# Kernel tuning notes

Hardware: AMD Instinct MI355X
Metric: run time of the kernel (lower is better)

## Reference

```python
import math
import jax, jax.numpy as jnp
import numpy as np

S = 4096          # total packed tokens (b*s with bsz=1)
NUM_HEADS = 16
HEAD_DIM = 80
SCALE = 1.0 / math.sqrt(HEAD_DIM)


def setup_inputs() -> dict:
    key = jax.random.key(0)
    kq, kk, kv = jax.random.split(key, 3)
    q = jax.random.normal(kq, (S, NUM_HEADS, HEAD_DIM), dtype=jnp.float32)
    k = jax.random.normal(kk, (S, NUM_HEADS, HEAD_DIM), dtype=jnp.float32)
    v = jax.random.normal(kv, (S, NUM_HEADS, HEAD_DIM), dtype=jnp.float32)
    # 4 packed sequences of 1024 tokens each (flatten_batch=True, bsz=1)
    cu_seqlens = jnp.array([0, 1024, 2048, 3072, 4096], dtype=jnp.int32)
    return {"q": q, "k": k, "v": v, "bsz": 1, "cu_seqlens": cu_seqlens}


def reference(q, k, v, bsz, cu_seqlens):
    # q/k/v: [(b s), h, d]; flatten_batch=True so bsz == 1
    s = q.shape[0] // bsz
    h, d = q.shape[1], q.shape[2]

    # Block-diagonal mask from cu_seqlens: True inside each packed sequence.
    seg = jnp.searchsorted(cu_seqlens[1:], jnp.arange(s), side="right")  # [s]
    mask = seg[:, None] == seg[None, :]                                  # [s, s]

    # '(b s) h d -> b h s d'
    qb = q.reshape(bsz, s, h, d).transpose(0, 2, 1, 3)
    kb = k.reshape(bsz, s, h, d).transpose(0, 2, 1, 3)
    vb = v.reshape(bsz, s, h, d).transpose(0, 2, 1, 3)

    scores = jnp.einsum("bhsd,bhtd->bhst", qb, kb) * SCALE
    bias = jnp.where(mask, jnp.zeros((), scores.dtype), jnp.finfo(scores.dtype).min)
    attn = jax.nn.softmax((scores + bias).astype(jnp.float32), axis=-1).astype(q.dtype)

    out = jnp.einsum("bhst,bhtd->bhsd", attn, vb)
    # 'b h s d -> (b s) h d'
    return out.transpose(0, 2, 1, 3).reshape(bsz * s, h, d)
```

## Files before the change

kernel.cpp:

```cpp
#include <hip/hip_runtime.h>
#include <hip/hip_bf16.h>
#include <math.h>

#define NTOK 4096
#define NH 16
#define HD 80
#define TOKSTRIDE (NH * HD)
#define QBLK 64
#define KVBLK 64
#define KSTR 80
#define VSTR 72
#define PSTR 72

typedef __bf16 bf16x4 __attribute__((ext_vector_type(4)));
typedef __bf16 bf16x8 __attribute__((ext_vector_type(8)));
typedef float  f32x4  __attribute__((ext_vector_type(4)));

__global__ __launch_bounds__(256)
void prepack(const float* __restrict__ qg, const float* __restrict__ kg,
             const float* __restrict__ vg, __bf16* __restrict__ qb,
             __bf16* __restrict__ kb, __bf16* __restrict__ vtb) {
  __shared__ __align__(16) __bf16 Vl[HD][VSTR];
  const int tid  = threadIdx.x;
  const int tok0 = blockIdx.x * 64;
  const int h    = blockIdx.y;
  const float qscale = 1.4426950408889634f / sqrtf((float)HD);

  for (int i = tid; i < 64 * 20; i += 256) {
    const int row = i / 20;
    const int c4  = (i % 20) * 4;
    const size_t gsrc = (size_t)(tok0 + row) * TOKSTRIDE + h * HD + c4;
    const size_t gdst = ((size_t)h * NTOK + tok0 + row) * HD + c4;

    float4 fq = *reinterpret_cast<const float4*>(qg + gsrc);
    bf16x4 uq;
    uq[0] = (__bf16)(fq.x * qscale); uq[1] = (__bf16)(fq.y * qscale);
    uq[2] = (__bf16)(fq.z * qscale); uq[3] = (__bf16)(fq.w * qscale);
    *reinterpret_cast<bf16x4*>(qb + gdst) = uq;

    float4 fk = *reinterpret_cast<const float4*>(kg + gsrc);
    bf16x4 uk;
    uk[0] = (__bf16)fk.x; uk[1] = (__bf16)fk.y;
    uk[2] = (__bf16)fk.z; uk[3] = (__bf16)fk.w;
    *reinterpret_cast<bf16x4*>(kb + gdst) = uk;

    float4 fv = *reinterpret_cast<const float4*>(vg + gsrc);
    Vl[c4 + 0][row] = (__bf16)fv.x; Vl[c4 + 1][row] = (__bf16)fv.y;
    Vl[c4 + 2][row] = (__bf16)fv.z; Vl[c4 + 3][row] = (__bf16)fv.w;
  }
  __syncthreads();
  for (int i = tid; i < HD * 8; i += 256) {
    const int d  = i / 8;
    const int c8 = (i % 8) * 8;
    bf16x8 val = *reinterpret_cast<const bf16x8*>(&Vl[d][c8]);
    *reinterpret_cast<bf16x8*>(vtb + ((size_t)h * HD + d) * NTOK + tok0 + c8) = val;
  }
}

__global__ __launch_bounds__(256, 4)
void vis_attn9(const __bf16* __restrict__ qb, const __bf16* __restrict__ kb,
               const __bf16* __restrict__ vtb, const int* __restrict__ cu,
               int n_cu, float* __restrict__ outg) {
  __shared__ __align__(16) unsigned char smem[31136];
  __bf16* Kl = reinterpret_cast<__bf16*>(smem);
  __bf16* Vt = reinterpret_cast<__bf16*>(smem + 10400);
  __bf16* Pl = reinterpret_cast<__bf16*>(smem + 21920);

  const int tid  = threadIdx.x;
  const int w    = tid >> 6;
  const int lane = tid & 63;
  const int lr   = lane & 15;
  const int g    = lane >> 4;

  const int q0 = blockIdx.x * QBLK;
  const int h  = blockIdx.y;

  int kv_start = 0, kv_end = NTOK;
  for (int i = 0; i + 1 < n_cu; ++i) {
    int a = cu[i], b = cu[i + 1];
    if (q0 >= a && q0 < b) { kv_start = a; kv_end = b; }
  }

  if (tid < 16) Kl[KVBLK * KSTR + tid] = (__bf16)0.0f;

  const int qrow = q0 + w * 16 + lr;
  const __bf16* qrptr = qb + ((size_t)h * NTOK + qrow) * HD;
  bf16x8 qf[3];
  #pragma unroll
  for (int c = 0; c < 3; ++c) {
    const int dbase = c * 32 + g * 8;
    if (dbase < HD) {
      qf[c] = *reinterpret_cast<const bf16x8*>(qrptr + dbase);
    } else {
      #pragma unroll
      for (int j = 0; j < 8; ++j) qf[c][j] = (__bf16)0.0f;
    }
  }

  bf16x8 vfl;
  {
    const __bf16 o = (lr == 0) ? (__bf16)1.0f : (__bf16)0.0f;
    #pragma unroll
    for (int j = 0; j < 8; ++j) vfl[j] = o;
  }

  f32x4 O[6];
  #pragma unroll
  for (int n = 0; n < 6; ++n) O[n] = (f32x4){0.f, 0.f, 0.f, 0.f};

  const __bf16* kbh  = kb  + (size_t)h * NTOK * HD;
  const __bf16* vtbh = vtb + (size_t)h * HD * NTOK;
  const char* gbase = reinterpret_cast<const char*>(kbh);
  const int vdelta = (int)(reinterpret_cast<const char*>(vtbh) - gbase);

  int goff[5], ginc[5], ldsoff[5];
  #pragma unroll
  for (int j = 0; j < 5; ++j) {
    const int c = tid + j * 256;
    if (c < 640) {
      const int row = c / 10, col = (c % 10) * 8;
      goff[j]   = (kv_start * HD + row * HD + col) * 2;
      ginc[j]   = KVBLK * HD * 2;
      ldsoff[j] = (row * KSTR + col) * 2;
    } else {
      const int c2 = c - 640, d = c2 / 8, kc = (c2 % 8) * 8;
      goff[j]   = vdelta + (kv_start + d * NTOK + kc) * 2;
      ginc[j]   = KVBLK * 2;
      ldsoff[j] = 10400 + (d * VSTR + kc) * 2;
    }
  }

  bf16x8 st[5];
  #pragma unroll
  for (int j = 0; j < 5; ++j) {
    st[j] = *reinterpret_cast<const bf16x8*>(gbase + goff[j]);
    goff[j] += ginc[j];
  }

  for (int kv0 = kv_start; kv0 < kv_end; kv0 += KVBLK) {
    __syncthreads();
    #pragma unroll
    for (int j = 0; j < 5; ++j)
      *reinterpret_cast<bf16x8*>(smem + ldsoff[j]) = st[j];
    __syncthreads();

    if (kv0 + KVBLK < kv_end) {
      #pragma unroll
      for (int j = 0; j < 5; ++j) {
        st[j] = *reinterpret_cast<const bf16x8*>(gbase + goff[j]);
        goff[j] += ginc[j];
      }
    }

    f32x4 S[4];
    __builtin_amdgcn_s_setprio(1);
    #pragma unroll
    for (int t = 0; t < 4; ++t) {
      S[t] = (f32x4){0.f, 0.f, 0.f, 0.f};
      #pragma unroll
      for (int c = 0; c < 3; ++c) {
        bf16x8 kf = *reinterpret_cast<const bf16x8*>(&Kl[(t * 16 + lr) * KSTR + c * 32 + g * 8]);
        S[t] = __builtin_amdgcn_mfma_f32_16x16x32_bf16(qf[c], kf, S[t], 0, 0, 0);
      }
    }
    __builtin_amdgcn_s_setprio(0);

    #pragma unroll
    for (int t = 0; t < 4; ++t) {
      #pragma unroll
      for (int r = 0; r < 4; ++r)
        S[t][r] = exp2f(S[t][r]);
    }

    #pragma unroll
    for (int t = 0; t < 4; ++t) {
      #pragma unroll
      for (int r = 0; r < 4; ++r)
        Pl[(w * 16 + g * 4 + r) * PSTR + t * 16 + lr] = (__bf16)S[t][r];
    }

    #pragma unroll
    for (int kc = 0; kc < 2; ++kc) {
      bf16x8 pf = *reinterpret_cast<const bf16x8*>(&Pl[(w * 16 + lr) * PSTR + kc * 32 + g * 8]);
      __builtin_amdgcn_s_setprio(1);
      #pragma unroll
      for (int n = 0; n < 5; ++n) {
        bf16x8 vf = *reinterpret_cast<const bf16x8*>(&Vt[(n * 16 + lr) * VSTR + kc * 32 + g * 8]);
        O[n] = __builtin_amdgcn_mfma_f32_16x16x32_bf16(pf, vf, O[n], 0, 0, 0);
      }
      O[5] = __builtin_amdgcn_mfma_f32_16x16x32_bf16(pf, vfl, O[5], 0, 0, 0);
      __builtin_amdgcn_s_setprio(0);
    }
  }

  float inv[4];
  #pragma unroll
  for (int r = 0; r < 4; ++r) {
    float l = __shfl(O[5][r], lane & 48);
    inv[r] = 1.0f / l;
  }
  const int orow0 = q0 + w * 16 + g * 4;
  #pragma unroll
  for (int n = 0; n < 5; ++n) {
    #pragma unroll
    for (int r = 0; r < 4; ++r)
      outg[(size_t)(orow0 + r) * TOKSTRIDE + h * HD + n * 16 + lr] = O[n][r] * inv[r];
  }
}

__global__ __launch_bounds__(256, 4)
void vis_attn_fb(const float* __restrict__ qg, const float* __restrict__ kg,
                 const float* __restrict__ vg, const int* __restrict__ cu,
                 int n_cu, float* __restrict__ outg) {
  __shared__ __align__(16) __bf16 Kl[KVBLK][104];
  __shared__ __align__(16) __bf16 Vt[HD][72];
  __shared__ __align__(16) __bf16 Pl[64][72];

  const int tid  = threadIdx.x;
  const int w    = tid >> 6;
  const int lane = tid & 63;
  const int lr   = lane & 15;
  const int g    = lane >> 4;
  const int q0 = blockIdx.x * 64;
  const int h  = blockIdx.y;

  int kv_start = 0, kv_end = NTOK;
  for (int i = 0; i + 1 < n_cu; ++i) {
    int a = cu[i], b = cu[i + 1];
    if (q0 >= a && q0 < b) { kv_start = a; kv_end = b; }
  }
  for (int i = tid; i < KVBLK * 16; i += 256)
    Kl[i >> 4][HD + (i & 15)] = (__bf16)0.0f;

  const float qscale = 1.4426950408889634f / sqrtf((float)HD);
  const int qrow = q0 + w * 16 + lr;
  const float* qptr = qg + (size_t)qrow * TOKSTRIDE + h * HD;
  bf16x8 qf[3];
  #pragma unroll
  for (int c = 0; c < 3; ++c) {
    const int dbase = c * 32 + g * 8;
    if (dbase < HD) {
      float4 f0 = *reinterpret_cast<const float4*>(qptr + dbase);
      float4 f1 = *reinterpret_cast<const float4*>(qptr + dbase + 4);
      qf[c][0] = (__bf16)(f0.x * qscale); qf[c][1] = (__bf16)(f0.y * qscale);
      qf[c][2] = (__bf16)(f0.z * qscale); qf[c][3] = (__bf16)(f0.w * qscale);
      qf[c][4] = (__bf16)(f1.x * qscale); qf[c][5] = (__bf16)(f1.y * qscale);
      qf[c][6] = (__bf16)(f1.z * qscale); qf[c][7] = (__bf16)(f1.w * qscale);
    } else {
      #pragma unroll
      for (int j = 0; j < 8; ++j) qf[c][j] = (__bf16)0.0f;
    }
  }

  f32x4 O[5];
  #pragma unroll
  for (int n = 0; n < 5; ++n) O[n] = (f32x4){0.f, 0.f, 0.f, 0.f};
  float m_run[4] = {-1e30f, -1e30f, -1e30f, -1e30f};
  float l_run[4] = {0.f, 0.f, 0.f, 0.f};

  for (int kv0 = kv_start; kv0 < kv_end; kv0 += KVBLK) {
    __syncthreads();
    for (int i = tid; i < KVBLK * (HD / 4); i += 256) {
      const int row = i / (HD / 4);
      const int c4  = (i % (HD / 4)) * 4;
      float4 f = *reinterpret_cast<const float4*>(
          kg + (size_t)(kv0 + row) * TOKSTRIDE + h * HD + c4);
      Kl[row][c4 + 0] = (__bf16)f.x; Kl[row][c4 + 1] = (__bf16)f.y;
      Kl[row][c4 + 2] = (__bf16)f.z; Kl[row][c4 + 3] = (__bf16)f.w;
    }
    for (int i = tid; i < KVBLK * (HD / 4); i += 256) {
      const int row = i / (HD / 4);
      const int c4  = (i % (HD / 4)) * 4;
      float4 f = *reinterpret_cast<const float4*>(
          vg + (size_t)(kv0 + row) * TOKSTRIDE + h * HD + c4);
      Vt[c4 + 0][row] = (__bf16)f.x; Vt[c4 + 1][row] = (__bf16)f.y;
      Vt[c4 + 2][row] = (__bf16)f.z; Vt[c4 + 3][row] = (__bf16)f.w;
    }
    __syncthreads();

    f32x4 S[4];
    #pragma unroll
    for (int t = 0; t < 4; ++t) {
      S[t] = (f32x4){0.f, 0.f, 0.f, 0.f};
      #pragma unroll
      for (int c = 0; c < 3; ++c) {
        bf16x8 kf = *reinterpret_cast<const bf16x8*>(&Kl[t * 16 + lr][c * 32 + g * 8]);
        S[t] = __builtin_amdgcn_mfma_f32_16x16x32_bf16(qf[c], kf, S[t], 0, 0, 0);
      }
    }
    float pmax[4];
    #pragma unroll
    for (int r = 0; r < 4; ++r)
      pmax[r] = fmaxf(fmaxf(S[0][r], S[1][r]), fmaxf(S[2][r], S[3][r]));
    #pragma unroll
    for (int r = 0; r < 4; ++r) {
      pmax[r] = fmaxf(pmax[r], __shfl_xor(pmax[r], 1));
      pmax[r] = fmaxf(pmax[r], __shfl_xor(pmax[r], 2));
      pmax[r] = fmaxf(pmax[r], __shfl_xor(pmax[r], 4));
      pmax[r] = fmaxf(pmax[r], __shfl_xor(pmax[r], 8));
    }
    float alpha[4];
    #pragma unroll
    for (int r = 0; r < 4; ++r) {
      float mn = fmaxf(m_run[r], pmax[r]);
      alpha[r] = exp2f(m_run[r] - mn);
      m_run[r] = mn;
    }
    #pragma unroll
    for (int t = 0; t < 4; ++t) {
      #pragma unroll
      for (int r = 0; r < 4; ++r)
        S[t][r] = exp2f(S[t][r] - m_run[r]);
    }
    float rsum[4];
    #pragma unroll
    for (int r = 0; r < 4; ++r) {
      rsum[r] = (S[0][r] + S[1][r]) + (S[2][r] + S[3][r]);
      rsum[r] += __shfl_xor(rsum[r], 1);
      rsum[r] += __shfl_xor(rsum[r], 2);
      rsum[r] += __shfl_xor(rsum[r], 4);
      rsum[r] += __shfl_xor(rsum[r], 8);
      l_run[r] = l_run[r] * alpha[r] + rsum[r];
    }
    #pragma unroll
    for (int n = 0; n < 5; ++n) {
      #pragma unroll
      for (int r = 0; r < 4; ++r) O[n][r] *= alpha[r];
    }
    #pragma unroll
    for (int t = 0; t < 4; ++t) {
      #pragma unroll
      for (int r = 0; r < 4; ++r)
        Pl[w * 16 + g * 4 + r][t * 16 + lr] = (__bf16)S[t][r];
    }
    #pragma unroll
    for (int kc = 0; kc < 2; ++kc) {
      bf16x8 pf = *reinterpret_cast<const bf16x8*>(&Pl[w * 16 + lr][kc * 32 + g * 8]);
      #pragma unroll
      for (int n = 0; n < 5; ++n) {
        bf16x8 vf = *reinterpret_cast<const bf16x8*>(&Vt[n * 16 + lr][kc * 32 + g * 8]);
        O[n] = __builtin_amdgcn_mfma_f32_16x16x32_bf16(pf, vf, O[n], 0, 0, 0);
      }
    }
  }

  float inv[4];
  #pragma unroll
  for (int r = 0; r < 4; ++r) inv[r] = 1.0f / l_run[r];
  const int orow0 = q0 + w * 16 + g * 4;
  #pragma unroll
  for (int n = 0; n < 5; ++n) {
    #pragma unroll
    for (int r = 0; r < 4; ++r)
      outg[(size_t)(orow0 + r) * TOKSTRIDE + h * HD + n * 16 + lr] = O[n][r] * inv[r];
  }
}

extern "C" void kernel_launch(void* const* d_in, const int* in_sizes, int n_in,
                              void* d_out, int out_size, void* d_ws, size_t ws_size,
                              hipStream_t stream) {
  const float* q  = (const float*)d_in[0];
  const float* k  = (const float*)d_in[1];
  const float* v  = (const float*)d_in[2];
  const int* cu   = (const int*)d_in[4];
  const int n_cu  = in_sizes[4];
  float* out      = (float*)d_out;

  const size_t one = (size_t)NH * NTOK * HD * sizeof(__bf16);

  if (ws_size >= 3 * one) {
    __bf16* qb  = (__bf16*)d_ws;
    __bf16* kb  = (__bf16*)((char*)d_ws + one);
    __bf16* vtb = (__bf16*)((char*)d_ws + 2 * one);
    dim3 gp(NTOK / 64, NH);
    prepack<<<gp, 256, 0, stream>>>(q, k, v, qb, kb, vtb);
    dim3 ga(NTOK / QBLK, NH);
    vis_attn9<<<ga, 256, 0, stream>>>(qb, kb, vtb, cu, n_cu, out);
  } else {
    dim3 gf(NTOK / 64, NH);
    vis_attn_fb<<<gf, 256, 0, stream>>>(q, k, v, cu, n_cu, out);
  }
}
```

Before: 64.26 us.

## Split KV tile across wave pairs and reduce partial outputs via LDS

New measurement: 65.12 us. No clear change (+1.3%).

```diff
diff --git a/kernel.cpp b/kernel.cpp
--- a/kernel.cpp
+++ b/kernel.cpp
@@ -57,17 +57,20 @@
   }
 }
 
-__global__ __launch_bounds__(256, 4)
-void vis_attn9(const __bf16* __restrict__ qb, const __bf16* __restrict__ kb,
-               const __bf16* __restrict__ vtb, const int* __restrict__ cu,
-               int n_cu, float* __restrict__ outg) {
+__global__ __launch_bounds__(512, 2)
+void vis_attn10(const __bf16* __restrict__ qb, const __bf16* __restrict__ kb,
+                const __bf16* __restrict__ vtb, const int* __restrict__ cu,
+                int n_cu, float* __restrict__ outg) {
   __shared__ __align__(16) unsigned char smem[31136];
   __bf16* Kl = reinterpret_cast<__bf16*>(smem);
   __bf16* Vt = reinterpret_cast<__bf16*>(smem + 10400);
   __bf16* Pl = reinterpret_cast<__bf16*>(smem + 21920);
+  float*  Cx = reinterpret_cast<float*>(smem);
 
   const int tid  = threadIdx.x;
   const int w    = tid >> 6;
+  const int wr   = w >> 1;
+  const int wc   = w & 1;
   const int lane = tid & 63;
   const int lr   = lane & 15;
   const int g    = lane >> 4;
@@ -83,7 +86,7 @@
 
   if (tid < 16) Kl[KVBLK * KSTR + tid] = (__bf16)0.0f;
 
-  const int qrow = q0 + w * 16 + lr;
+  const int qrow = q0 + wr * 16 + lr;
   const __bf16* qrptr = qb + ((size_t)h * NTOK + qrow) * HD;
   bf16x8 qf[3];
   #pragma unroll
@@ -113,98 +116,114 @@
   const char* gbase = reinterpret_cast<const char*>(kbh);
   const int vdelta = (int)(reinterpret_cast<const char*>(vtbh) - gbase);
 
-  int goff[5], ginc[5], ldsoff[5];
-  #pragma unroll
-  for (int j = 0; j < 5; ++j) {
-    const int c = tid + j * 256;
+  int goff[3], ginc[3], ldsoff[3];
+  #pragma unroll
+  for (int j = 0; j < 3; ++j) {
+    const int c = tid + j * 512;
     if (c < 640) {
       const int row = c / 10, col = (c % 10) * 8;
       goff[j]   = (kv_start * HD + row * HD + col) * 2;
       ginc[j]   = KVBLK * HD * 2;
       ldsoff[j] = (row * KSTR + col) * 2;
-    } else {
+    } else if (c < 1280) {
       const int c2 = c - 640, d = c2 / 8, kc = (c2 % 8) * 8;
       goff[j]   = vdelta + (kv_start + d * NTOK + kc) * 2;
       ginc[j]   = KVBLK * 2;
       ldsoff[j] = 10400 + (d * VSTR + kc) * 2;
-    }
-  }
-
-  bf16x8 st[5];
-  #pragma unroll
-  for (int j = 0; j < 5; ++j) {
-    st[j] = *reinterpret_cast<const bf16x8*>(gbase + goff[j]);
-    goff[j] += ginc[j];
+    } else {
+      goff[j] = 0; ginc[j] = 0; ldsoff[j] = 0;
+    }
+  }
+  const bool j2 = (tid < 256);
+
+  bf16x8 st[3];
+  #pragma unroll
+  for (int j = 0; j < 3; ++j) {
+    if (j < 2 || j2) {
+      st[j] = *reinterpret_cast<const bf16x8*>(gbase + goff[j]);
+      goff[j] += ginc[j];
+    }
   }
 
   for (int kv0 = kv_start; kv0 < kv_end; kv0 += KVBLK) {
     __syncthreads();
     #pragma unroll
-    for (int j = 0; j < 5; ++j)
-      *reinterpret_cast<bf16x8*>(smem + ldsoff[j]) = st[j];
+    for (int j = 0; j < 3; ++j)
+      if (j < 2 || j2)
+        *reinterpret_cast<bf16x8*>(smem + ldsoff[j]) = st[j];
     __syncthreads();
 
     if (kv0 + KVBLK < kv_end) {
       #pragma unroll
-      for (int j = 0; j < 5; ++j) {
-        st[j] = *reinterpret_cast<const bf16x8*>(gbase + goff[j]);
-        goff[j] += ginc[j];
+      for (int j = 0; j < 3; ++j) {
+        if (j < 2 || j2) {
+          st[j] = *reinterpret_cast<const bf16x8*>(gbase + goff[j]);
+          goff[j] += ginc[j];
+        }
       }
     }
 
-    f32x4 S[4];
+    f32x4 S[2];
     __builtin_amdgcn_s_setprio(1);
     #pragma unroll
-    for (int t = 0; t < 4; ++t) {
+    for (int t = 0; t < 2; ++t) {
       S[t] = (f32x4){0.f, 0.f, 0.f, 0.f};
       #pragma unroll
       for (int c = 0; c < 3; ++c) {
-        bf16x8 kf = *reinterpret_cast<const bf16x8*>(&Kl[(t * 16 + lr) * KSTR + c * 32 + g * 8]);
+        bf16x8 kf = *reinterpret_cast<const bf16x8*>(
+            &Kl[(wc * 32 + t * 16 + lr) * KSTR + c * 32 + g * 8]);
         S[t] = __builtin_amdgcn_mfma_f32_16x16x32_bf16(qf[c], kf, S[t], 0, 0, 0);
       }
     }
     __builtin_amdgcn_s_setprio(0);
 
     #pragma unroll
-    for (int t = 0; t < 4; ++t) {
+    for (int t = 0; t < 2; ++t) {
       #pragma unroll
       for (int r = 0; r < 4; ++r)
-        S[t][r] = exp2f(S[t][r]);
-    }
-
-    #pragma unroll
-    for (int t = 0; t < 4; ++t) {
+        Pl[(wr * 16 + g * 4 + r) * PSTR + wc * 32 + t * 16 + lr] =
+            (__bf16)exp2f(S[t][r]);
+    }
+
+    bf16x8 pf = *reinterpret_cast<const bf16x8*>(
+        &Pl[(wr * 16 + lr) * PSTR + wc * 32 + g * 8]);
+    __builtin_amdgcn_s_setprio(1);
+    #pragma unroll
+    for (int n = 0; n < 5; ++n) {
+      bf16x8 vf = *reinterpret_cast<const bf16x8*>(
+          &Vt[(n * 16 + lr) * VSTR + wc * 32 + g * 8]);
+      O[n] = __builtin_amdgcn_mfma_f32_16x16x32_bf16(pf, vf, O[n], 0, 0, 0);
+    }
+    O[5] = __builtin_amdgcn_mfma_f32_16x16x32_bf16(pf, vfl, O[5], 0, 0, 0);
+    __builtin_amdgcn_s_setprio(0);
+  }
+
+  __syncthreads();
+  if (wc == 1) {
+    #pragma unroll
+    for (int n = 0; n < 6; ++n)
+      *reinterpret_cast<f32x4*>(&Cx[((wr * 6 + n) * 64 + lane) * 4]) = O[n];
+  }
+  __syncthreads();
+  if (wc == 0) {
+    #pragma unroll
+    for (int n = 0; n < 6; ++n) {
+      f32x4 p = *reinterpret_cast<const f32x4*>(&Cx[((wr * 6 + n) * 64 + lane) * 4]);
+      O[n] += p;
+    }
+    float inv[4];
+    #pragma unroll
+    for (int r = 0; r < 4; ++r) {
+      float l = __shfl(O[5][r], lane & 48);
+      inv[r] = 1.0f / l;
+    }
+    const int orow0 = q0 + wr * 16 + g * 4;
+    #pragma unroll
+    for (int n = 0; n < 5; ++n) {
       #pragma unroll
       for (int r = 0; r < 4; ++r)
-        Pl[(w * 16 + g * 4 + r) * PSTR + t * 16 + lr] = (__bf16)S[t][r];
-    }
-
-    #pragma unroll
-    for (int kc = 0; kc < 2; ++kc) {
-      bf16x8 pf = *reinterpret_cast<const bf16x8*>(&Pl[(w * 16 + lr) * PSTR + kc * 32 + g * 8]);
-      __builtin_amdgcn_s_setprio(1);
-      #pragma unroll
-      for (int n = 0; n < 5; ++n) {
-        bf16x8 vf = *reinterpret_cast<const bf16x8*>(&Vt[(n * 16 + lr) * VSTR + kc * 32 + g * 8]);
-        O[n] = __builtin_amdgcn_mfma_f32_16x16x32_bf16(pf, vf, O[n], 0, 0, 0);
-      }
-      O[5] = __builtin_amdgcn_mfma_f32_16x16x32_bf16(pf, vfl, O[5], 0, 0, 0);
-      __builtin_amdgcn_s_setprio(0);
-    }
-  }
-
-  float inv[4];
-  #pragma unroll
-  for (int r = 0; r < 4; ++r) {
-    float l = __shfl(O[5][r], lane & 48);
-    inv[r] = 1.0f / l;
-  }
-  const int orow0 = q0 + w * 16 + g * 4;
-  #pragma unroll
-  for (int n = 0; n < 5; ++n) {
-    #pragma unroll
-    for (int r = 0; r < 4; ++r)
-      outg[(size_t)(orow0 + r) * TOKSTRIDE + h * HD + n * 16 + lr] = O[n][r] * inv[r];
+        outg[(size_t)(orow0 + r) * TOKSTRIDE + h * HD + n * 16 + lr] = O[n][r] * inv[r];
+    }
   }
 }
 
@@ -375,7 +394,7 @@
     dim3 gp(NTOK / 64, NH);
     prepack<<<gp, 256, 0, stream>>>(q, k, v, qb, kb, vtb);
     dim3 ga(NTOK / QBLK, NH);
-    vis_attn9<<<ga, 256, 0, stream>>>(qb, kb, vtb, cu, n_cu, out);
+    vis_attn10<<<ga, 512, 0, stream>>>(qb, kb, vtb, cu, n_cu, out);
   } else {
     dim3 gf(NTOK / 64, NH);
     vis_attn_fb<<<gf, 256, 0, stream>>>(q, k, v, cu, n_cu, out);
```

## Keep softmax probabilities in registers by transposing QK^T MFMA operands

Applied to the files above, without the earlier changes.

After: 63.33 us. Within noise of the previous version (-1.4%).

```diff
diff --git a/kernel.cpp b/kernel.cpp
--- a/kernel.cpp
+++ b/kernel.cpp
@@ -15,6 +15,24 @@
 typedef __bf16 bf16x4 __attribute__((ext_vector_type(4)));
 typedef __bf16 bf16x8 __attribute__((ext_vector_type(8)));
 typedef float  f32x4  __attribute__((ext_vector_type(4)));
+typedef short  short4v __attribute__((ext_vector_type(4)));
+
+#if __has_builtin(__builtin_amdgcn_mfma_f32_16x16x16bf16_1k)
+__device__ inline f32x4 mfma16(bf16x4 a, bf16x4 b, f32x4 c) {
+  return __builtin_amdgcn_mfma_f32_16x16x16bf16_1k(
+      __builtin_bit_cast(short4v, a), __builtin_bit_cast(short4v, b), c, 0, 0, 0);
+}
+#elif __has_builtin(__builtin_amdgcn_mfma_f32_16x16x16_bf16)
+__device__ inline f32x4 mfma16(bf16x4 a, bf16x4 b, f32x4 c) {
+  return __builtin_amdgcn_mfma_f32_16x16x16_bf16(a, b, c, 0, 0, 0);
+}
+#else
+__device__ inline f32x4 mfma16(bf16x4 a, bf16x4 b, f32x4 c) {
+  asm volatile("v_mfma_f32_16x16x16_bf16 %0, %1, %2, %0"
+               : "+v"(c) : "v"(a), "v"(b));
+  return c;
+}
+#endif
 
 __global__ __launch_bounds__(256)
 void prepack(const float* __restrict__ qg, const float* __restrict__ kg,
@@ -58,13 +76,12 @@
 }
 
 __global__ __launch_bounds__(256, 4)
-void vis_attn9(const __bf16* __restrict__ qb, const __bf16* __restrict__ kb,
-               const __bf16* __restrict__ vtb, const int* __restrict__ cu,
-               int n_cu, float* __restrict__ outg) {
-  __shared__ __align__(16) unsigned char smem[31136];
+void vis_attn11(const __bf16* __restrict__ qb, const __bf16* __restrict__ kb,
+                const __bf16* __restrict__ vtb, const int* __restrict__ cu,
+                int n_cu, float* __restrict__ outg) {
+  __shared__ __align__(16) unsigned char smem[21920];
   __bf16* Kl = reinterpret_cast<__bf16*>(smem);
   __bf16* Vt = reinterpret_cast<__bf16*>(smem + 10400);
-  __bf16* Pl = reinterpret_cast<__bf16*>(smem + 21920);
 
   const int tid  = threadIdx.x;
   const int w    = tid >> 6;
@@ -97,12 +114,9 @@
     }
   }
 
-  bf16x8 vfl;
-  {
-    const __bf16 o = (lr == 0) ? (__bf16)1.0f : (__bf16)0.0f;
-    #pragma unroll
-    for (int j = 0; j < 8; ++j) vfl[j] = o;
-  }
+  bf16x4 vfl;
+  #pragma unroll
+  for (int j = 0; j < 4; ++j) vfl[j] = (lr == 0) ? (__bf16)1.0f : (__bf16)0.0f;
 
   f32x4 O[6];
   #pragma unroll
@@ -152,45 +166,35 @@
       }
     }
 
-    f32x4 S[4];
+    bf16x4 pf[4];
     __builtin_amdgcn_s_setprio(1);
     #pragma unroll
     for (int t = 0; t < 4; ++t) {
-      S[t] = (f32x4){0.f, 0.f, 0.f, 0.f};
+      f32x4 S = (f32x4){0.f, 0.f, 0.f, 0.f};
       #pragma unroll
       for (int c = 0; c < 3; ++c) {
         bf16x8 kf = *reinterpret_cast<const bf16x8*>(&Kl[(t * 16 + lr) * KSTR + c * 32 + g * 8]);
-        S[t] = __builtin_amdgcn_mfma_f32_16x16x32_bf16(qf[c], kf, S[t], 0, 0, 0);
-      }
+        S = __builtin_amdgcn_mfma_f32_16x16x32_bf16(kf, qf[c], S, 0, 0, 0);
+      }
+      #pragma unroll
+      for (int r = 0; r < 4; ++r)
+        pf[t][r] = (__bf16)exp2f(S[r]);
     }
     __builtin_amdgcn_s_setprio(0);
 
-    #pragma unroll
-    for (int t = 0; t < 4; ++t) {
-      #pragma unroll
-      for (int r = 0; r < 4; ++r)
-        S[t][r] = exp2f(S[t][r]);
-    }
-
-    #pragma unroll
-    for (int t = 0; t < 4; ++t) {
-      #pragma unroll
-      for (int r = 0; r < 4; ++r)
-        Pl[(w * 16 + g * 4 + r) * PSTR + t * 16 + lr] = (__bf16)S[t][r];
-    }
-
-    #pragma unroll
-    for (int kc = 0; kc < 2; ++kc) {
-      bf16x8 pf = *reinterpret_cast<const bf16x8*>(&Pl[(w * 16 + lr) * PSTR + kc * 32 + g * 8]);
-      __builtin_amdgcn_s_setprio(1);
-      #pragma unroll
-      for (int n = 0; n < 5; ++n) {
-        bf16x8 vf = *reinterpret_cast<const bf16x8*>(&Vt[(n * 16 + lr) * VSTR + kc * 32 + g * 8]);
-        O[n] = __builtin_amdgcn_mfma_f32_16x16x32_bf16(pf, vf, O[n], 0, 0, 0);
-      }
-      O[5] = __builtin_amdgcn_mfma_f32_16x16x32_bf16(pf, vfl, O[5], 0, 0, 0);
-      __builtin_amdgcn_s_setprio(0);
-    }
+    __builtin_amdgcn_s_setprio(1);
+    #pragma unroll
+    for (int n = 0; n < 5; ++n) {
+      #pragma unroll
+      for (int t = 0; t < 4; ++t) {
+        bf16x4 vf = *reinterpret_cast<const bf16x4*>(&Vt[(n * 16 + lr) * VSTR + t * 16 + g * 4]);
+        O[n] = mfma16(pf[t], vf, O[n]);
+      }
+    }
+    #pragma unroll
+    for (int t = 0; t < 4; ++t)
+      O[5] = mfma16(pf[t], vfl, O[5]);
+    __builtin_amdgcn_s_setprio(0);
   }
 
   float inv[4];
@@ -375,7 +379,7 @@
     dim3 gp(NTOK / 64, NH);
     prepack<<<gp, 256, 0, stream>>>(q, k, v, qb, kb, vtb);
     dim3 ga(NTOK / QBLK, NH);
-    vis_attn9<<<ga, 256, 0, stream>>>(qb, kb, vtb, cu, n_cu, out);
+    vis_attn11<<<ga, 256, 0, stream>>>(qb, kb, vtb, cu, n_cu, out);
   } else {
     dim3 gf(NTOK / 64, NH);
     vis_attn_fb<<<gf, 256, 0, stream>>>(q, k, v, cu, n_cu, out);
```
